# Performance work log

Hardware: AMD Instinct MI355X
Metric: run time of the kernel (lower is better)

The kernel has to match this reference:

```python
import jax, jax.numpy as jnp
import numpy as np

B, S, N, C, D = 1, 6, 10000, 128, 4
HEADS, PTS = 4, 8
HF, WF = 28, 50
M = HF * WF


def setup_inputs() -> dict:
    key0 = jax.random.key(0)
    ks = jax.random.split(key0, 14)
    sc = C ** -0.5
    d = {}
    d["query"] = jax.random.normal(ks[0], (B, N, C), jnp.float32)
    d["key"] = jax.random.normal(ks[1], (S, M, B, C), jnp.float32)
    d["value"] = jax.random.normal(ks[2], (S, M, B, C), jnp.float32)
    d["query_pos"] = jax.random.normal(ks[3], (B, N, C), jnp.float32) * 0.1
    d["reference_points_cam"] = jax.random.uniform(ks[4], (S, B, N, D, 2), jnp.float32, -0.2, 1.2)
    d["bev_mask"] = jax.random.randint(ks[5], (S, B, N, D), 0, 2).astype(bool)
    d["w_off"] = jax.random.normal(ks[6], (C, HEADS * PTS * 2), jnp.float32) * sc
    d["b_off"] = jax.random.normal(ks[7], (HEADS * PTS * 2,), jnp.float32) * 0.01
    d["w_attn"] = jax.random.normal(ks[8], (C, HEADS * PTS), jnp.float32) * sc
    d["b_attn"] = jax.random.normal(ks[9], (HEADS * PTS,), jnp.float32) * 0.01
    d["w_val"] = jax.random.normal(ks[10], (C, C), jnp.float32) * sc
    d["b_val"] = jax.random.normal(ks[11], (C,), jnp.float32) * 0.01
    d["w_out"] = jax.random.normal(ks[12], (C, C), jnp.float32) * sc
    d["b_out"] = jax.random.normal(ks[13], (C,), jnp.float32) * 0.01
    d["Hf"] = HF
    d["Wf"] = WF
    return d


def reference(query, key, value, query_pos, reference_points_cam, bev_mask,
              w_off, b_off, w_attn, b_attn, w_val, b_val, w_out, b_out, Hf, Wf):
    # SpatialCrossAttention with MSDeformAttn3D (BEVFormer semantics, eval mode: dropout=identity).
    # The torch data-dependent gather/rebatch/scatter is replaced by mathematically equivalent
    # masked computation: deformable attention is per-query independent, so running it for all
    # BEV queries per camera and mask-accumulating yields identical slots.
    B_, N_, C_ = query.shape
    S_ = key.shape[0]
    D_ = reference_points_cam.shape[3]
    H, P = HEADS, PTS
    dh = C_ // H
    Pd = P // D_
    q = query + query_pos  # (B,N,C)
    off = (q @ w_off + b_off).reshape(B_, N_, H, Pd, D_, 2)
    aw = jax.nn.softmax((q @ w_attn + b_attn).reshape(B_, N_, H, P), axis=-1)  # over levels*points (L=1)
    # value projection; per-camera feature maps laid out as (B,S,H,Hf*Wf,dh)
    v = jnp.transpose(value, (2, 0, 1, 3))  # (B,S,M,C)
    v = v @ w_val + b_val
    v = v.reshape(B_, S_, Hf * Wf, H, dh).transpose(0, 1, 3, 2, 4)  # (B,S,H,M,dh)
    ref = jnp.transpose(reference_points_cam, (1, 0, 2, 3, 4))  # (B,S,N,D,2)
    norm = jnp.array([Wf, Hf], jnp.float32)  # offset_normalizer = (W, H)
    loc = ref[:, :, :, None, None, :, :] + off[:, None] / norm  # (B,S,N,H,Pd,D,2)
    loc = loc.reshape(B_, S_, N_, H, P, 2)
    # bilinear sampling, zero padding, align_corners=False
    ix = loc[..., 0] * Wf - 0.5
    iy = loc[..., 1] * Hf - 0.5
    x0 = jnp.floor(ix)
    y0 = jnp.floor(iy)

    def flat(a):  # (B,S,N,H,P) -> (B,S,H,N*P)
        return a.transpose(0, 1, 3, 2, 4).reshape(B_, S_, H, N_ * P)

    def gather(xi, yi):
        ok = (xi >= 0) & (xi < Wf) & (yi >= 0) & (yi < Hf)
        xi_c = jnp.clip(xi, 0, Wf - 1).astype(jnp.int32)
        yi_c = jnp.clip(yi, 0, Hf - 1).astype(jnp.int32)
        idx = flat(yi_c * Wf + xi_c)
        g = jnp.take_along_axis(v, idx[..., None], axis=3)  # (B,S,H,N*P,dh)
        return g * flat(ok.astype(v.dtype))[..., None]

    wx1 = ix - x0
    wy1 = iy - y0
    wx0 = 1.0 - wx1
    wy0 = 1.0 - wy1
    samp = (gather(x0, y0) * flat(wx0 * wy0)[..., None]
            + gather(x0 + 1, y0) * flat(wx1 * wy0)[..., None]
            + gather(x0, y0 + 1) * flat(wx0 * wy1)[..., None]
            + gather(x0 + 1, y0 + 1) * flat(wx1 * wy1)[..., None])  # (B,S,H,N*P,dh)
    samp = samp.reshape(B_, S_, H, N_, P, dh)
    out = jnp.einsum('bshnpd,bnhp->bsnhd', samp, aw).reshape(B_, S_, N_, C_)
    # masked scatter-accumulate back to BEV slots
    mask = jnp.transpose(jnp.any(bev_mask, axis=-1), (1, 0, 2))  # (B,S,N)
    slots = jnp.sum(out * mask[..., None].astype(out.dtype), axis=1)  # (B,N,C)
    count = jnp.maximum(mask.astype(out.dtype).sum(axis=1), 1.0)
    slots = slots / count[..., None]
    return slots @ w_out + b_out + query  # dropout is identity in eval
```

## Files before the change

### kernel.cpp

```cpp
#include <hip/hip_runtime.h>
#include <math.h>

#define S_ 6
#define N_ 10000
#define C_ 128
#define D_ 4
#define H_ 4
#define P_ 8
#define HF_ 28
#define WF_ 50
#define M_ (HF_ * WF_)
#define DH_ 32
#define SM_ (S_ * M_)
#define QB_ 4

#define NB_V ((SM_ + 31) / 32)
#define NB_O ((N_ + 31) / 32)

typedef float floatx2 __attribute__((ext_vector_type(2)));

template <int NC, int MT, int MR, int MODE>
__device__ __forceinline__ void gemm_body(
    const float* __restrict__ A, const float* __restrict__ A2,
    const float* __restrict__ B0, const float* __restrict__ B1,
    const float* __restrict__ bias0, const float* __restrict__ bias1,
    float* __restrict__ outf, char* __restrict__ out8,
    int Mrows, int m0, int tid, int nthreads, float (*Alds)[132]) {
  constexpr int NTHR = (NC / 4) * (MT / MR);

  for (int i = tid; i < MT * 32; i += nthreads) {
    int r = i >> 5, k = (i & 31) * 4;
    int row = m0 + r;
    float4 v = make_float4(0.f, 0.f, 0.f, 0.f);
    if (row < Mrows) {
      v = *(const float4*)(A + (size_t)row * C_ + k);
      if (MODE == 1) {
        float4 v2 = *(const float4*)(A2 + (size_t)row * C_ + k);
        v.x += v2.x; v.y += v2.y; v.z += v2.z; v.w += v2.w;
      }
    }
    *(float4*)(&Alds[r][k]) = v;
  }
  __syncthreads();
  if (tid >= NTHR) return;

  int ci = tid % (NC / 4);
  int mi = tid / (NC / 4);
  int c0 = ci * 4, r0 = mi * MR;

  const float* bs;
  if (MODE == 1) bs = (c0 < 64) ? bias0 + c0 : bias1 + (c0 - 64);
  else bs = bias0 + c0;

  float acc[MR][4];
#pragma unroll
  for (int j = 0; j < MR; ++j)
#pragma unroll
    for (int cc = 0; cc < 4; ++cc) acc[j][cc] = bs[cc];

#pragma unroll 2
  for (int k4 = 0; k4 < C_; k4 += 4) {
    float bf[16];
#pragma unroll
    for (int kk = 0; kk < 4; ++kk) {
      int k = k4 + kk;
      float4 b4;
      if (MODE == 1)
        b4 = (c0 < 64) ? *(const float4*)(B0 + (size_t)k * 64 + c0)
                       : *(const float4*)(B1 + (size_t)k * 32 + (c0 - 64));
      else
        b4 = *(const float4*)(B0 + (size_t)k * NC + c0);
      bf[kk * 4 + 0] = b4.x; bf[kk * 4 + 1] = b4.y;
      bf[kk * 4 + 2] = b4.z; bf[kk * 4 + 3] = b4.w;
    }
    float af[MR * 4];
#pragma unroll
    for (int j = 0; j < MR; ++j) {
      float4 a4 = *(const float4*)(&Alds[r0 + j][k4]);
      af[j * 4 + 0] = a4.x; af[j * 4 + 1] = a4.y;
      af[j * 4 + 2] = a4.z; af[j * 4 + 3] = a4.w;
    }
#pragma unroll
    for (int j = 0; j < MR; ++j)
#pragma unroll
      for (int kk = 0; kk < 4; ++kk)
#pragma unroll
        for (int cc = 0; cc < 4; ++cc)
          acc[j][cc] = fmaf(af[j * 4 + kk], bf[kk * 4 + cc], acc[j][cc]);
  }

#pragma unroll
  for (int j = 0; j < MR; ++j) {
    int row = m0 + r0 + j;
    if (row >= Mrows) continue;
    if (MODE == 0) {
      int s = row / M_, mm = row % M_;
      int h = c0 >> 5, d0 = c0 & 31;
      int w = __builtin_amdgcn_cvt_pk_fp8_f32(acc[j][0], acc[j][1], 0, false);
      w = __builtin_amdgcn_cvt_pk_fp8_f32(acc[j][2], acc[j][3], w, true);
      *(int*)(out8 + (((size_t)s * H_ + h) * M_ + mm) * 32 + d0) = w;
    } else if (MODE == 1) {
      *(float4*)(outf + (size_t)row * 96 + c0) =
          make_float4(acc[j][0], acc[j][1], acc[j][2], acc[j][3]);
    } else {
      float4 qv = *(const float4*)(A2 + (size_t)row * C_ + c0);
      *(float4*)(outf + (size_t)row * C_ + c0) =
          make_float4(acc[j][0] + qv.x, acc[j][1] + qv.y,
                      acc[j][2] + qv.z, acc[j][3] + qv.w);
    }
  }
}

__global__ __launch_bounds__(256) void prep_kernel(
    const float* __restrict__ value, const float* __restrict__ w_val,
    const float* __restrict__ b_val, char* __restrict__ vh8,
    const float* __restrict__ query, const float* __restrict__ query_pos,
    const float* __restrict__ w_off, const float* __restrict__ b_off,
    const float* __restrict__ w_attn, const float* __restrict__ b_attn,
    float* __restrict__ OFFL) {
  __shared__ float Alds[32][132];
  int bid = blockIdx.x;
  if (bid < NB_V) {
    gemm_body<128, 32, 4, 0>(value, nullptr, w_val, nullptr, b_val, nullptr,
                             nullptr, vh8, SM_, bid * 32, threadIdx.x, 256,
                             Alds);
  } else {
    gemm_body<96, 32, 4, 1>(query, query_pos, w_off, w_attn, b_off, b_attn,
                            OFFL, nullptr, N_, (bid - NB_V) * 32, threadIdx.x,
                            256, Alds);
  }
}

__global__ __launch_bounds__(256) void out_kernel(
    const float* __restrict__ slots, const float* __restrict__ query,
    const float* __restrict__ w_out, const float* __restrict__ b_out,
    float* __restrict__ out) {
  __shared__ float Alds[16][132];
  gemm_body<128, 16, 2, 2>(slots, query, w_out, nullptr, b_out, nullptr,
                           out, nullptr, N_, blockIdx.x * 16, threadIdx.x,
                           256, Alds);
}

__global__ __launch_bounds__(128) void attn2_kernel(
    const float* __restrict__ OFFL,
    const float* __restrict__ refpts,
    const int*   __restrict__ bev_mask,
    const char*  __restrict__ vh8,
    float* __restrict__ slots) {
  int n0 = blockIdx.x * QB_;
  int tid = threadIdx.x;

  __shared__ float off[QB_][64];
  __shared__ float logits[QB_][32];
  __shared__ float aw[QB_][32];
  __shared__ float refl[QB_][48];
  __shared__ int smask[QB_][6];
  __shared__ int2 sidx[QB_][194];
  __shared__ float4 sw[QB_][194];

  for (int i = tid; i < QB_ * 96; i += 128) {
    int q = i / 96, c = i % 96;
    float v = OFFL[(size_t)(n0 + q) * 96 + c];
    if (c < 64) off[q][c] = v; else logits[q][c - 64] = v;
  }
  for (int i = tid; i < QB_ * 48; i += 128) {
    int q = i / 48, rem = i % 48;
    int s = rem >> 3, r8 = rem & 7;
    refl[q][rem] = refpts[((size_t)s * N_ + (n0 + q)) * 8 + r8];
  }
  if (tid < QB_ * 6) {
    int q = tid / 6, s = tid % 6;
    const int* bm = bev_mask + ((size_t)s * N_ + (n0 + q)) * D_;
    smask[q][s] = (bm[0] | bm[1] | bm[2] | bm[3]) ? 1 : 0;
  }
  __syncthreads();

  {
    int q = tid >> 5, j = tid & 31, h = j >> 3;
    float mx = -1e30f;
#pragma unroll
    for (int p = 0; p < P_; ++p) mx = fmaxf(mx, logits[q][h * P_ + p]);
    float sum = 0.f;
#pragma unroll
    for (int p = 0; p < P_; ++p) sum += expf(logits[q][h * P_ + p] - mx);
    aw[q][j] = expf(logits[q][j] - mx) / sum;
  }
  __syncthreads();

  for (int i = tid; i < QB_ * 192; i += 128) {
    int q = i / 192, j = i % 192;
    int s = j >> 5, w32 = j & 31, p = w32 >> 2, h = w32 & 3;
    int pd = p >> 2, dd = p & 3;
    float rx = refl[q][s * 8 + dd * 2 + 0];
    float ry = refl[q][s * 8 + dd * 2 + 1];
    float ox = off[q][h * 16 + pd * 8 + dd * 2 + 0];
    float oy = off[q][h * 16 + pd * 8 + dd * 2 + 1];
    float ix = rx * (float)WF_ + ox - 0.5f;
    float iy = ry * (float)HF_ + oy - 0.5f;
    float x0f = floorf(ix), y0f = floorf(iy);
    int x0 = (int)x0f, y0 = (int)y0f;
    float wx1 = ix - x0f, wy1 = iy - y0f;
    float wx0 = 1.f - wx1, wy0 = 1.f - wy1;
    float a = aw[q][h * P_ + p];
    bool vx0 = (x0 >= 0) && (x0 < WF_);
    bool vx1 = (x0 + 1 >= 0) && (x0 + 1 < WF_);
    bool vy0 = (y0 >= 0) && (y0 < HF_);
    bool vy1 = (y0 + 1 >= 0) && (y0 + 1 < HF_);
    int y0c = min(max(y0, 0), HF_ - 1);
    int y1c = min(max(y0 + 1, 0), HF_ - 1);
    int xb = min(max(x0, -1), WF_ - 1);
    int base = (s * H_ + h) * M_;
    int itop = (base + y0c * WF_ + xb) * 32;
    int ibot = (base + y1c * WF_ + xb) * 32;
    float w00 = (vx0 && vy0) ? wx0 * wy0 * a : 0.f;
    float w10 = (vx1 && vy0) ? wx1 * wy0 * a : 0.f;
    float w01 = (vx0 && vy1) ? wx0 * wy1 * a : 0.f;
    float w11 = (vx1 && vy1) ? wx1 * wy1 * a : 0.f;
    sidx[q][j] = make_int2(itop, ibot);
    sw[q][j] = make_float4(w00, w10, w01, w11);
  }
  __syncthreads();

  int q = tid >> 5, t = tid & 31, h = t >> 3, c8 = t & 7;
  bool hi = (c8 & 4) != 0;
  const char* vb = vh8 + c8 * 8;
  float av[8] = {0.f, 0.f, 0.f, 0.f, 0.f, 0.f, 0.f, 0.f};
  for (int s = 0; s < S_; ++s) {
    if (!smask[q][s]) continue;
#pragma unroll
    for (int p = 0; p < P_; ++p) {
      int j = s * 32 + p * 4 + h;
      int2 I = sidx[q][j];
      float4 W = sw[q][j];
      float wt = hi ? W.y : W.x;
      float wb = hi ? W.w : W.z;
      int2 ta = *(const int2*)(vb + I.x);
      int2 tb = *(const int2*)(vb + I.y);
      floatx2 t0 = __builtin_amdgcn_cvt_pk_f32_fp8(ta.x, false);
      floatx2 t1 = __builtin_amdgcn_cvt_pk_f32_fp8(ta.x, true);
      floatx2 t2 = __builtin_amdgcn_cvt_pk_f32_fp8(ta.y, false);
      floatx2 t3 = __builtin_amdgcn_cvt_pk_f32_fp8(ta.y, true);
      av[0] = fmaf(t0.x, wt, av[0]); av[1] = fmaf(t0.y, wt, av[1]);
      av[2] = fmaf(t1.x, wt, av[2]); av[3] = fmaf(t1.y, wt, av[3]);
      av[4] = fmaf(t2.x, wt, av[4]); av[5] = fmaf(t2.y, wt, av[5]);
      av[6] = fmaf(t3.x, wt, av[6]); av[7] = fmaf(t3.y, wt, av[7]);
      floatx2 b0 = __builtin_amdgcn_cvt_pk_f32_fp8(tb.x, false);
      floatx2 b1 = __builtin_amdgcn_cvt_pk_f32_fp8(tb.x, true);
      floatx2 b2 = __builtin_amdgcn_cvt_pk_f32_fp8(tb.y, false);
      floatx2 b3 = __builtin_amdgcn_cvt_pk_f32_fp8(tb.y, true);
      av[0] = fmaf(b0.x, wb, av[0]); av[1] = fmaf(b0.y, wb, av[1]);
      av[2] = fmaf(b1.x, wb, av[2]); av[3] = fmaf(b1.y, wb, av[3]);
      av[4] = fmaf(b2.x, wb, av[4]); av[5] = fmaf(b2.y, wb, av[5]);
      av[6] = fmaf(b3.x, wb, av[6]); av[7] = fmaf(b3.y, wb, av[7]);
    }
  }
#pragma unroll
  for (int k = 0; k < 8; ++k) av[k] += __shfl_xor(av[k], 4);

  if (!hi) {
    int cnt = smask[q][0] + smask[q][1] + smask[q][2] +
              smask[q][3] + smask[q][4] + smask[q][5];
    float inv = 1.f / (float)(cnt > 0 ? cnt : 1);
    float* dst = slots + (size_t)(n0 + q) * C_ + h * DH_ + (c8 & 3) * 8;
    *(float4*)dst = make_float4(av[0] * inv, av[1] * inv,
                                av[2] * inv, av[3] * inv);
    *(float4*)(dst + 4) = make_float4(av[4] * inv, av[5] * inv,
                                      av[6] * inv, av[7] * inv);
  }
}

extern "C" void kernel_launch(void* const* d_in, const int* in_sizes, int n_in,
                              void* d_out, int out_size, void* d_ws, size_t ws_size,
                              hipStream_t stream) {
  const float* query     = (const float*)d_in[0];
  const float* value     = (const float*)d_in[2];
  const float* query_pos = (const float*)d_in[3];
  const float* refpts    = (const float*)d_in[4];
  const int*   bev_mask  = (const int*)d_in[5];
  const float* w_off     = (const float*)d_in[6];
  const float* b_off     = (const float*)d_in[7];
  const float* w_attn    = (const float*)d_in[8];
  const float* b_attn    = (const float*)d_in[9];
  const float* w_val     = (const float*)d_in[10];
  const float* b_val     = (const float*)d_in[11];
  const float* w_out     = (const float*)d_in[12];
  const float* b_out     = (const float*)d_in[13];

  char* ws = (char*)d_ws;
  char* vh8   = ws + 64;
  float* OFFL = (float*)(ws + 2150400);
  float* slots = (float*)(ws + 5990400);

  prep_kernel<<<NB_V + NB_O, 256, 0, stream>>>(
      value, w_val, b_val, vh8, query, query_pos, w_off, b_off, w_attn, b_attn,
      OFFL);
  attn2_kernel<<<N_ / QB_, 128, 0, stream>>>(OFFL, refpts, bev_mask, vh8,
                                             slots);
  out_kernel<<<(N_ + 15) / 16, 256, 0, stream>>>(
      slots, query, w_out, b_out, (float*)d_out);
}
```

Before: 157.7 us.

## Fuse output projection into attention kernel and add odd-x shifted value copy

Folds the output projection, bias and residual into the attention kernel: each block writes its per-query slots to shared memory and computes the 128x128 matvec there, so the slots buffer round trip and the third kernel launch go away. The value-projection epilogue also writes a second fp8 copy laid out as odd-x column pairs, so a bilinear tap starting at an odd x can read both columns from one aligned 64-byte-strided location. This costs extra writes and workspace in the prep kernel. The fused matvec re-reads w_out from global memory in every block with only 4 queries per block, which may cost more than the separate GEMM did.

```diff
diff --git a/kernel.cpp b/kernel.cpp
--- a/kernel.cpp
+++ b/kernel.cpp
@@ -13,6 +13,7 @@
 #define DH_ 32
 #define SM_ (S_ * M_)
 #define QB_ 4
+#define ABYTES (S_ * H_ * M_ * 32)
 
 #define NB_V ((SM_ + 31) / 32)
 #define NB_O ((N_ + 31) / 32)
@@ -95,18 +96,20 @@
     if (row >= Mrows) continue;
     if (MODE == 0) {
       int s = row / M_, mm = row % M_;
+      int y = mm / WF_, x = mm % WF_;
       int h = c0 >> 5, d0 = c0 & 31;
       int w = __builtin_amdgcn_cvt_pk_fp8_f32(acc[j][0], acc[j][1], 0, false);
       w = __builtin_amdgcn_cvt_pk_fp8_f32(acc[j][2], acc[j][3], w, true);
-      *(int*)(out8 + (((size_t)s * H_ + h) * M_ + mm) * 32 + d0) = w;
+      size_t hm = (size_t)s * H_ + h;
+      *(int*)(out8 + (hm * M_ + mm) * 32 + d0) = w;
+      if (x > 0) {
+        int kp = (x - 1) >> 1, slot = 1 - (x & 1);
+        *(int*)(out8 + ABYTES + ((hm * HF_ + y) * 25 + kp) * 64 +
+                slot * 32 + d0) = w;
+      }
     } else if (MODE == 1) {
       *(float4*)(outf + (size_t)row * 96 + c0) =
           make_float4(acc[j][0], acc[j][1], acc[j][2], acc[j][3]);
-    } else {
-      float4 qv = *(const float4*)(A2 + (size_t)row * C_ + c0);
-      *(float4*)(outf + (size_t)row * C_ + c0) =
-          make_float4(acc[j][0] + qv.x, acc[j][1] + qv.y,
-                      acc[j][2] + qv.z, acc[j][3] + qv.w);
     }
   }
 }
@@ -131,22 +134,15 @@
   }
 }
 
-__global__ __launch_bounds__(256) void out_kernel(
-    const float* __restrict__ slots, const float* __restrict__ query,
-    const float* __restrict__ w_out, const float* __restrict__ b_out,
-    float* __restrict__ out) {
-  __shared__ float Alds[16][132];
-  gemm_body<128, 16, 2, 2>(slots, query, w_out, nullptr, b_out, nullptr,
-                           out, nullptr, N_, blockIdx.x * 16, threadIdx.x,
-                           256, Alds);
-}
-
 __global__ __launch_bounds__(128) void attn2_kernel(
     const float* __restrict__ OFFL,
     const float* __restrict__ refpts,
     const int*   __restrict__ bev_mask,
     const char*  __restrict__ vh8,
-    float* __restrict__ slots) {
+    const float* __restrict__ query,
+    const float* __restrict__ w_out,
+    const float* __restrict__ b_out,
+    float* __restrict__ out) {
   int n0 = blockIdx.x * QB_;
   int tid = threadIdx.x;
 
@@ -157,6 +153,7 @@
   __shared__ int smask[QB_][6];
   __shared__ int2 sidx[QB_][194];
   __shared__ float4 sw[QB_][194];
+  __shared__ float sl[QB_][130];
 
   for (int i = tid; i < QB_ * 96; i += 128) {
     int q = i / 96, c = i % 96;
@@ -208,10 +205,21 @@
     bool vy1 = (y0 + 1 >= 0) && (y0 + 1 < HF_);
     int y0c = min(max(y0, 0), HF_ - 1);
     int y1c = min(max(y0 + 1, 0), HF_ - 1);
-    int xb = min(max(x0, -1), WF_ - 1);
-    int base = (s * H_ + h) * M_;
-    int itop = (base + y0c * WF_ + xb) * 32;
-    int ibot = (base + y1c * WF_ + xb) * 32;
+    int hm = s * H_ + h;
+    int itop, ibot;
+    if (x0 >= 0 && x0 <= WF_ - 2 && !(x0 & 1)) {
+      itop = (hm * M_ + y0c * WF_ + x0) * 32;
+      ibot = (hm * M_ + y1c * WF_ + x0) * 32;
+    } else if (x0 >= 1 && x0 <= WF_ - 1 && (x0 & 1)) {
+      int kp = (x0 - 1) >> 1;
+      itop = ABYTES + ((hm * HF_ + y0c) * 25 + kp) * 64;
+      ibot = ABYTES + ((hm * HF_ + y1c) * 25 + kp) * 64;
+    } else if (x0 == -1) {
+      itop = (hm * M_ + y0c * WF_) * 32 - 32;
+      ibot = (hm * M_ + y1c * WF_) * 32 - 32;
+    } else {
+      itop = ibot = 0;
+    }
     float w00 = (vx0 && vy0) ? wx0 * wy0 * a : 0.f;
     float w10 = (vx1 && vy0) ? wx1 * wy0 * a : 0.f;
     float w01 = (vx0 && vy1) ? wx0 * wy1 * a : 0.f;
@@ -261,11 +269,27 @@
     int cnt = smask[q][0] + smask[q][1] + smask[q][2] +
               smask[q][3] + smask[q][4] + smask[q][5];
     float inv = 1.f / (float)(cnt > 0 ? cnt : 1);
-    float* dst = slots + (size_t)(n0 + q) * C_ + h * DH_ + (c8 & 3) * 8;
-    *(float4*)dst = make_float4(av[0] * inv, av[1] * inv,
-                                av[2] * inv, av[3] * inv);
-    *(float4*)(dst + 4) = make_float4(av[4] * inv, av[5] * inv,
-                                      av[6] * inv, av[7] * inv);
+    float* dst = &sl[q][h * DH_ + (c8 & 3) * 8];
+#pragma unroll
+    for (int k = 0; k < 8; ++k) dst[k] = av[k] * inv;
+  }
+  __syncthreads();
+
+  {
+    int q2 = tid >> 5, c0 = (tid & 31) * 4;
+    int n = n0 + q2;
+    float4 qv = *(const float4*)(query + (size_t)n * C_ + c0);
+    float4 bv = *(const float4*)(b_out + c0);
+    float r0 = bv.x + qv.x, r1 = bv.y + qv.y;
+    float r2 = bv.z + qv.z, r3 = bv.w + qv.w;
+#pragma unroll 4
+    for (int k = 0; k < C_; ++k) {
+      float a = sl[q2][k];
+      float4 w4 = *(const float4*)(w_out + (size_t)k * C_ + c0);
+      r0 = fmaf(a, w4.x, r0); r1 = fmaf(a, w4.y, r1);
+      r2 = fmaf(a, w4.z, r2); r3 = fmaf(a, w4.w, r3);
+    }
+    *(float4*)(out + (size_t)n * C_ + c0) = make_float4(r0, r1, r2, r3);
   }
 }
 
@@ -288,14 +312,12 @@
 
   char* ws = (char*)d_ws;
   char* vh8   = ws + 64;
-  float* OFFL = (float*)(ws + 2150400);
-  float* slots = (float*)(ws + 5990400);
+  float* OFFL = (float*)(ws + 64 + 2 * (size_t)ABYTES + 64);
 
   prep_kernel<<<NB_V + NB_O, 256, 0, stream>>>(
       value, w_val, b_val, vh8, query, query_pos, w_off, b_off, w_attn, b_attn,
       OFFL);
   attn2_kernel<<<N_ / QB_, 128, 0, stream>>>(OFFL, refpts, bev_mask, vh8,
-                                             slots);
-  out_kernel<<<(N_ + 15) / 16, 256, 0, stream>>>(
-      slots, query, w_out, b_out, (float*)d_out);
+                                             query, w_out, b_out,
+                                             (float*)d_out);
 }
```

After: 159.1 us. No clear change (+0.9%).

## Add odd-aligned pair-packed fp8 value copy and store bilinear weights as fp16

Applied to the files above, without the earlier changes.

The value projection now also writes a second fp8 copy laid out as horizontally adjacent pixel pairs starting at odd x. The sampler can then pick, for any x0, a layout where the 64-byte x0/x0+1 pair is contiguous and aligned. Bilinear weights in shared memory are stored as fp16 instead of fp32, halving that LDS footprint and read traffic. In exchange the prep kernel does extra global writes, the workspace grows, and fp16 weights lose some precision.

```diff
diff --git a/kernel.cpp b/kernel.cpp
--- a/kernel.cpp
+++ b/kernel.cpp
@@ -13,11 +13,13 @@
 #define DH_ 32
 #define SM_ (S_ * M_)
 #define QB_ 4
+#define ABYTES (S_ * H_ * M_ * 32)
 
 #define NB_V ((SM_ + 31) / 32)
 #define NB_O ((N_ + 31) / 32)
 
 typedef float floatx2 __attribute__((ext_vector_type(2)));
+typedef _Float16 half4v __attribute__((ext_vector_type(4)));
 
 template <int NC, int MT, int MR, int MODE>
 __device__ __forceinline__ void gemm_body(
@@ -95,10 +97,17 @@
     if (row >= Mrows) continue;
     if (MODE == 0) {
       int s = row / M_, mm = row % M_;
+      int y = mm / WF_, x = mm % WF_;
       int h = c0 >> 5, d0 = c0 & 31;
       int w = __builtin_amdgcn_cvt_pk_fp8_f32(acc[j][0], acc[j][1], 0, false);
       w = __builtin_amdgcn_cvt_pk_fp8_f32(acc[j][2], acc[j][3], w, true);
-      *(int*)(out8 + (((size_t)s * H_ + h) * M_ + mm) * 32 + d0) = w;
+      size_t hm = (size_t)s * H_ + h;
+      *(int*)(out8 + (hm * M_ + mm) * 32 + d0) = w;
+      if (x > 0) {
+        int kp = (x - 1) >> 1, slot = 1 - (x & 1);
+        *(int*)(out8 + ABYTES + ((hm * HF_ + y) * 25 + kp) * 64 +
+                slot * 32 + d0) = w;
+      }
     } else if (MODE == 1) {
       *(float4*)(outf + (size_t)row * 96 + c0) =
           make_float4(acc[j][0], acc[j][1], acc[j][2], acc[j][3]);
@@ -156,7 +165,7 @@
   __shared__ float refl[QB_][48];
   __shared__ int smask[QB_][6];
   __shared__ int2 sidx[QB_][194];
-  __shared__ float4 sw[QB_][194];
+  __shared__ half4v swh[QB_][194];
 
   for (int i = tid; i < QB_ * 96; i += 128) {
     int q = i / 96, c = i % 96;
@@ -208,16 +217,28 @@
     bool vy1 = (y0 + 1 >= 0) && (y0 + 1 < HF_);
     int y0c = min(max(y0, 0), HF_ - 1);
     int y1c = min(max(y0 + 1, 0), HF_ - 1);
-    int xb = min(max(x0, -1), WF_ - 1);
-    int base = (s * H_ + h) * M_;
-    int itop = (base + y0c * WF_ + xb) * 32;
-    int ibot = (base + y1c * WF_ + xb) * 32;
+    int hm = s * H_ + h;
+    int itop, ibot;
+    if (x0 >= 0 && x0 <= WF_ - 2 && !(x0 & 1)) {
+      itop = (hm * M_ + y0c * WF_ + x0) * 32;
+      ibot = (hm * M_ + y1c * WF_ + x0) * 32;
+    } else if (x0 >= 1 && x0 <= WF_ - 1 && (x0 & 1)) {
+      int kp = (x0 - 1) >> 1;
+      itop = ABYTES + ((hm * HF_ + y0c) * 25 + kp) * 64;
+      ibot = ABYTES + ((hm * HF_ + y1c) * 25 + kp) * 64;
+    } else if (x0 == -1) {
+      itop = (hm * M_ + y0c * WF_) * 32 - 32;
+      ibot = (hm * M_ + y1c * WF_) * 32 - 32;
+    } else {
+      itop = ibot = 0;
+    }
     float w00 = (vx0 && vy0) ? wx0 * wy0 * a : 0.f;
     float w10 = (vx1 && vy0) ? wx1 * wy0 * a : 0.f;
     float w01 = (vx0 && vy1) ? wx0 * wy1 * a : 0.f;
     float w11 = (vx1 && vy1) ? wx1 * wy1 * a : 0.f;
     sidx[q][j] = make_int2(itop, ibot);
-    sw[q][j] = make_float4(w00, w10, w01, w11);
+    half4v wv = {(_Float16)w00, (_Float16)w10, (_Float16)w01, (_Float16)w11};
+    swh[q][j] = wv;
   }
   __syncthreads();
 
@@ -231,9 +252,9 @@
     for (int p = 0; p < P_; ++p) {
       int j = s * 32 + p * 4 + h;
       int2 I = sidx[q][j];
-      float4 W = sw[q][j];
-      float wt = hi ? W.y : W.x;
-      float wb = hi ? W.w : W.z;
+      half4v W = swh[q][j];
+      float wt = hi ? (float)W[1] : (float)W[0];
+      float wb = hi ? (float)W[3] : (float)W[2];
       int2 ta = *(const int2*)(vb + I.x);
       int2 tb = *(const int2*)(vb + I.y);
       floatx2 t0 = __builtin_amdgcn_cvt_pk_f32_fp8(ta.x, false);
@@ -287,9 +308,9 @@
   const float* b_out     = (const float*)d_in[13];
 
   char* ws = (char*)d_ws;
-  char* vh8   = ws + 64;
-  float* OFFL = (float*)(ws + 2150400);
-  float* slots = (float*)(ws + 5990400);
+  char* vh8    = ws + 64;
+  float* OFFL  = (float*)(ws + 64 + 2 * (size_t)ABYTES + 64);
+  float* slots = (float*)(ws + 64 + 2 * (size_t)ABYTES + 64 + 3840000);
 
   prep_kernel<<<NB_V + NB_O, 256, 0, stream>>>(
       value, w_val, b_val, vh8, query, query_pos, w_off, b_off, w_attn, b_attn,
```

Result: no change. 158.5 us (+0.5%).
